# Performance work log

Hardware: AMD Instinct MI355X
Metric: run time of the kernel (lower is better)

Reference implementation:

```python
import jax, jax.numpy as jnp
import numpy as np

jax.config.update("jax_enable_x64", True)

SIGMA = 10            # STDP time window
POPULATIONS = 2
LR = 1e-3
IN_FEATURES = 1568    # populations * 28 * 28
OUT_FEATURES = 10
BATCH = 64
NUM_STEPS = 256
TWO_SIGMA = 2 * SIGMA


def _normalize(LL, prior):
    # clamp to [-7, 0], then log-normalize over population axis / over outputs
    LL = jnp.clip(LL, -7.0, 0.0)
    pf = LL.reshape(POPULATIONS, -1, OUT_FEATURES)
    LL = (pf - jax.nn.logsumexp(pf, axis=0, keepdims=True)).reshape(IN_FEATURES, OUT_FEATURES)
    prior = jnp.clip(prior, -7.0, 0.0)
    prior = prior - jax.nn.logsumexp(prior)
    return LL, prior


def _run(x, LL, prior):
    B, T, F = x.shape
    LL = LL.astype(jnp.float64)
    prior = prior.astype(jnp.float64)
    LL, prior = _normalize(LL, prior)  # __init__ calls normalize_probs()
    # Padded cumulative spike counts: Cp[:, t] = sum_{s < t} x[:, s]
    Cp = jnp.concatenate(
        [jnp.zeros((B, 1, F), jnp.int32), jnp.cumsum(x.astype(jnp.int32), axis=1)], axis=1)
    t = jnp.arange(T)
    lo = jnp.take(Cp, jnp.clip(t - SIGMA + 1, 0, T), axis=1)   # sum_{s <= t-sigma} x, (B,T,F)
    tp_sigma = jnp.take(Cp, t + 1, axis=1) - lo                # LTP trace: spikes in [t-sigma+1, t]
    tp_s2inf = lo                                              # LTD trace: spikes older than sigma
    potential = tp_sigma > 0                                   # OR of binary spikes in sigma-window
    # post_only gate: no presynaptic spike in [t+1-4*sigma, t-1]
    no_pre = (jnp.take(Cp, t, axis=1)
              - jnp.take(Cp, jnp.clip(t + 1 - 4 * SIGMA, 0, T), axis=1)) == 0

    xs = (jnp.moveaxis(x, 1, 0), jnp.moveaxis(potential, 1, 0),
          jnp.moveaxis(tp_sigma, 1, 0), jnp.moveaxis(tp_s2inf, 1, 0),
          jnp.moveaxis(no_pre, 1, 0), t)

    dt = LL.dtype
    ring0 = jnp.zeros((TWO_SIGMA, B, OUT_FEATURES), jnp.int32)
    z0 = jnp.zeros((B, OUT_FEATURES), jnp.int32)
    carry0 = (LL, prior, jnp.asarray(1.0, dt), ring0, z0, z0, jax.random.key(42))

    def step(carry, inp):
        LL, prior, decay, ring, ring_sum, cum, key = carry
        x_t, pot_t, tps_t, tps2_t, nopre_t, tt = inp
        key, sk = jax.random.split(key)
        logits = pot_t.astype(dt) @ LL + prior                  # (B, out)
        w = jax.nn.one_hot(jax.random.categorical(sk, logits, axis=-1),
                           OUT_FEATURES, dtype=dt)              # sampled winners (B, out)
        tpost = ring_sum.astype(dt)                             # post trace, winners in [t-2sig, t-1]
        tpost_inf = (cum - ring_sum).astype(dt)                 # post trace, older than 2*sigma
        ltp = jnp.einsum('bi,bo->io', tps_t.astype(dt), w)
        ltd = jnp.einsum('bi,bo->io', tps2_t.astype(dt), w)
        post_pre = jnp.einsum('bi,bo->io', x_t.astype(dt), tpost)
        post_only = jnp.einsum('bi,bo->io', nopre_t.astype(dt), tpost_inf)
        scale = LR / decay
        LL = LL + ((jnp.exp(-LL) - 1.0) * ltp - ltd - post_pre - post_only) * scale
        ps = w.sum(axis=0)
        prior = prior + ((jnp.exp(-prior) - 1.0) * ps - (1.0 - ps)) * scale
        LL, prior = _normalize(LL, prior)
        wi = w.astype(jnp.int32)
        slot = tt % TWO_SIGMA
        ring_sum = ring_sum + wi - ring[slot]
        ring = ring.at[slot].set(wi)
        cum = cum + wi
        return (LL, prior, decay + 1.0, ring, ring_sum, cum, key), wi

    (LL, prior, *_), winners = jax.lax.scan(step, carry0, xs)
    return winners, LL, prior


def setup_inputs():
    key = jax.random.key(0)
    k1, k2, k3 = jax.random.split(key, 3)
    x = jax.random.randint(k1, (BATCH, NUM_STEPS, IN_FEATURES), 0, 2, dtype=jnp.int32)
    log_likelihood = jax.random.uniform(k2, (IN_FEATURES, OUT_FEATURES), dtype=jnp.float64) * -1.0 - 1.0
    log_prior = jax.random.uniform(k3, (OUT_FEATURES,), dtype=jnp.float64) * -1.0 - 1.0
    return {"x": x, "log_likelihood": log_likelihood, "log_prior": log_prior}


def reference(x, log_likelihood, log_prior):
    winners, _, _ = _run(x, log_likelihood, log_prior)
    return jnp.argmax(winners.sum(axis=0), axis=-1)  # (batch,), as in the torch forward
```

## Files before the change

### kernel.cpp

```cpp
#include <hip/hip_runtime.h>
#include <stdint.h>
#include <math.h>

#define NF 1568
#define PPOP 784
#define NOUT 10
#define NB 64
#define NT 256
#define RINGN 20
#define NBLK 8
#define TPB 512
#define PSH 98
#define TSW 16
#define TCH 64
#define ICH 64
#define LDP 66

__device__ __forceinline__ uint32_t rotl32(uint32_t v, int r){ return (v<<r)|(v>>(32-r)); }

__device__ __forceinline__ void tf2x32(uint32_t k0, uint32_t k1, uint32_t x0, uint32_t x1,
                                       uint32_t& o0, uint32_t& o1){
  uint32_t ks2 = k0 ^ k1 ^ 0x1BD11BDAu;
  x0 += k0; x1 += k1;
#define TF_RND(r) { x0 += x1; x1 = rotl32(x1,(r)); x1 ^= x0; }
  TF_RND(13) TF_RND(15) TF_RND(26) TF_RND(6)
  x0 += k1;  x1 += ks2 + 1u;
  TF_RND(17) TF_RND(29) TF_RND(16) TF_RND(24)
  x0 += ks2; x1 += k0 + 2u;
  TF_RND(13) TF_RND(15) TF_RND(26) TF_RND(6)
  x0 += k0;  x1 += k1 + 3u;
  TF_RND(17) TF_RND(29) TF_RND(16) TF_RND(24)
  x0 += k1;  x1 += ks2 + 4u;
  TF_RND(13) TF_RND(15) TF_RND(26) TF_RND(6)
  x0 += ks2; x1 += k0 + 5u;
#undef TF_RND
  o0 = x0; o1 = x1;
}

__global__ void kInit(const float* __restrict__ prior_in, double* __restrict__ prior,
                      uint32_t* __restrict__ sk){
  int tid = threadIdx.x;
  if (tid == 0){
    uint32_t k0 = 0u, k1 = 42u;
    for (int t = 0; t < NT; t++){
      uint32_t a,b; tf2x32(k0,k1,0u,1u,a,b); sk[2*t] = a; sk[2*t+1] = b;
      uint32_t c,d; tf2x32(k0,k1,0u,0u,c,d); k0 = c; k1 = d;
    }
  }
  if (tid == 1){
    double v[NOUT];
    double m = -1e300;
    for (int o = 0; o < NOUT; o++){
      double p = (double)prior_in[o];
      p = fmin(0.0, fmax(-7.0, p));
      v[o] = p; m = fmax(m, p);
    }
    double s = 0.0;
    for (int o = 0; o < NOUT; o++) s += exp(v[o]-m);
    double lse = log(s) + m;
    for (int o = 0; o < NOUT; o++) prior[o] = v[o] - lse;
  }
}

__global__ void kInitLL(const float* __restrict__ LL_in, double* __restrict__ G){
  int u = blockIdx.x*256 + threadIdx.x;
  int p = u/NOUT, o = u%NOUT;
  if (p >= PPOP) return;
  double l0 = fmin(0.0, fmax(-7.0, (double)LL_in[p*NOUT+o]));
  double l1 = fmin(0.0, fmax(-7.0, (double)LL_in[(p+PPOP)*NOUT+o]));
  double m = fmax(l0,l1);
  double lse = log(exp(l0-m)+exp(l1-m)) + m;
  G[o*NF + p]        = l0 - lse;
  G[o*NF + p + PPOP] = l1 - lse;
}

__global__ void kTraceC(const int* __restrict__ x, uint16_t* __restrict__ stage,
                        uint64_t* __restrict__ hist_st, int* __restrict__ tot_st, int t0){
  int b = blockIdx.y;
  int i = blockIdx.x*256 + threadIdx.x;
  if (i >= NF) return;
  int sidx = b*NF + i;
  uint64_t hist = (t0 == 0) ? 0ull : hist_st[sidx];
  int total     = (t0 == 0) ? 0    : tot_st[sidx];
  const int* xb = x + (size_t)b*NT*NF + i;
  for (int tl = 0; tl < TCH; tl++){
    int t = t0 + tl;
    int xv = xb[(size_t)t*NF];
    hist = (hist << 1) | (uint64_t)(uint32_t)xv;
    total += xv;
    int tps  = __popcll(hist & 0x3FFull);
    int tps2 = total - tps;
    int pot  = (tps > 0) ? 1 : 0;
    int npre = ((hist & 0x000000FFFFFFFFFEull) == 0) ? 1 : 0;
    stage[((size_t)tl*NB + b)*NF + i] =
      (uint16_t)(tps | (tps2<<4) | (pot<<12) | (npre<<13) | (xv<<14));
  }
  hist_st[sidx] = hist; tot_st[sidx] = total;
}

__global__ void kPack(const uint16_t* __restrict__ stage, uint64_t* __restrict__ masks, int t0){
  __shared__ uint16_t ld[NB*LDP];
  int tl = blockIdx.y, chunk = blockIdx.x;
  int i0 = chunk*ICH;
  int tid = threadIdx.x, lane = tid & 63, wv = tid >> 6;
  for (int r = wv; r < NB; r += 4){
    int i = i0 + lane;
    ld[r*LDP + lane] = (i < NF) ? stage[((size_t)tl*NB + r)*NF + i] : (uint16_t)0;
  }
  __syncthreads();
  int t = t0 + tl;
  for (int r = 0; r < 16; r++){
    int il = wv*16 + r;
    int i = i0 + il;
    if (i >= NF) break;
    uint16_t v = ld[lane*LDP + il];
    uint64_t sel = 0;
#pragma unroll
    for (int k = 0; k < 15; k++){
      uint64_t m = __ballot(((v >> k) & 1) != 0);
      if (lane == k) sel = m;
    }
    if (lane < 15) masks[((size_t)t*16 + lane)*NF + i] = sel;
  }
}

__global__ void kGum(const uint32_t* __restrict__ sk, double* __restrict__ gum){
  int t = blockIdx.x;
  uint32_t k0 = sk[2*t], k1 = sk[2*t+1];
  for (int idx = threadIdx.x; idx < NB*NOUT; idx += blockDim.x){
    uint32_t h,l; tf2x32(k0,k1,0u,(uint32_t)idx,h,l);
    uint64_t bits = ((uint64_t)h << 32) | (uint64_t)l;
    uint64_t fb = (bits >> 12) | 0x3FF0000000000000ull;
    double u01 = __longlong_as_double((long long)fb) - 1.0;
    double u = fmax(2.2250738585072014e-308, u01);
    gum[(size_t)t*NB*NOUT + idx] = -log(-log(u));
  }
}

__device__ __forceinline__ uint32_t poll32(uint64_t* addr, uint32_t tag){
  for (;;){
    uint64_t v = __hip_atomic_load(addr, __ATOMIC_RELAXED, __HIP_MEMORY_SCOPE_AGENT);
    if ((uint32_t)(v >> 32) == tag) return (uint32_t)v;
    __builtin_amdgcn_s_sleep(1);
  }
}

__device__ __forceinline__ int shpix(int s, int j){
  return s*PSH + (j < PSH ? j : j + (PPOP - PSH));
}

__global__ void __launch_bounds__(TPB)
kFused(const uint64_t* __restrict__ masks, double* __restrict__ G,
       const double* __restrict__ prior_g, const double* __restrict__ gum,
       uint64_t* part_lo, uint64_t* part_hi, uint64_t* wslots,
       int* __restrict__ out){
  const int bid = blockIdx.x, tid = threadIdx.x;
  const int lane = tid & 63, wv = tid >> 6;

  __shared__ double LL_s[NOUT][NF];
  __shared__ uint64_t scratch[14*196];
  __shared__ double pin_s[NBLK][NOUT];
  __shared__ double red_s[8][NOUT];
  __shared__ double colsum_s[NOUT], shsum_s[NOUT];
  __shared__ double prior_s[NOUT], pv_s[NOUT];
  __shared__ double lse_sh;
  __shared__ uint64_t wm_s[NOUT];
  __shared__ uint64_t ring_s[RINGN*NOUT];
  __shared__ uint64_t TP_s[NOUT][5];
  __shared__ int ring_cnt_s[NB*NOUT];
  __shared__ int cum_s[NB*NOUT];
  __shared__ int wloc_s[8];
  __shared__ uint32_t pk_s[NBLK];
  __shared__ int wlist_s[8][64];

  uint64_t* pot_s = scratch;
  uint64_t* bst   = scratch;

  double* LLf = &LL_s[0][0];
  for (int k = tid; k < NOUT*NF; k += TPB) LLf[k] = G[k];
  if (tid < NOUT) prior_s[tid] = prior_g[tid];
  for (int k = tid; k < RINGN*NOUT; k += TPB) ring_s[k] = 0;
  for (int k = tid; k < NB*NOUT; k += TPB){ ring_cnt_s[k] = 0; cum_s[k] = 0; }
  __syncthreads();

  for (int t = 0; t < NT; t++){
    const uint32_t tag = (uint32_t)(t + 1);
    const int b = bid*8 + wv;
    const uint64_t* M0 = masks + (size_t)t*16*NF;
    const uint64_t* potrow = M0 + 12*NF;

    double gpre = (lane < NOUT) ? gum[((size_t)t*NB + b)*NOUT + lane] : 0.0;

    if (t == 0){
      double a0=0,a1=0,a2=0,a3=0,a4=0,a5=0,a6=0,a7=0,a8=0,a9=0;
      for (int i = tid; i < NF; i += TPB){
        a0+=LL_s[0][i]; a1+=LL_s[1][i]; a2+=LL_s[2][i]; a3+=LL_s[3][i]; a4+=LL_s[4][i];
        a5+=LL_s[5][i]; a6+=LL_s[6][i]; a7+=LL_s[7][i]; a8+=LL_s[8][i]; a9+=LL_s[9][i];
      }
#define WRED(x) for (int s = 32; s > 0; s >>= 1) x += __shfl_down(x, s, 64);
      WRED(a0) WRED(a1) WRED(a2) WRED(a3) WRED(a4)
      WRED(a5) WRED(a6) WRED(a7) WRED(a8) WRED(a9)
      if (lane == 0){
        red_s[wv][0]=a0; red_s[wv][1]=a1; red_s[wv][2]=a2; red_s[wv][3]=a3;
        red_s[wv][4]=a4; red_s[wv][5]=a5; red_s[wv][6]=a6; red_s[wv][7]=a7;
        red_s[wv][8]=a8; red_s[wv][9]=a9;
      }
      __syncthreads();
      if (tid < NOUT){
        double s = 0.0;
        for (int w8 = 0; w8 < 8; w8++) s += red_s[w8][tid];
        colsum_s[tid] = s;
      }
      __syncthreads();
      for (int k = tid; k < NF; k += TPB) pot_s[k] = potrow[k];
      __syncthreads();
    } else {
      if (tid < NBLK*NOUT){
        uint32_t lo = poll32(&part_lo[tid], (uint32_t)t);
        uint32_t hi = poll32(&part_hi[tid], (uint32_t)t);
        pin_s[tid/NOUT][tid%NOUT] = __longlong_as_double(((uint64_t)hi << 32) | lo);
      } else if (tid >= 128){
        for (int k = tid - 128; k < NF; k += (TPB - 128)) pot_s[k] = potrow[k];
      }
      __syncthreads();
      if (tid < NOUT){
        double s = 0.0;
        for (int w8 = 0; w8 < NBLK; w8++) s += pin_s[w8][tid];
        colsum_s[tid] = s;
      }
      if (t < TSW){
        for (int s = 0; s < NBLK; s++){
          if (s == bid) continue;
          for (int k = tid; k < 2*PSH*NOUT; k += TPB){
            int o = k/(2*PSH), r = k%(2*PSH);
            int i = shpix(s, r);
            LL_s[o][i] = __hip_atomic_load(&G[o*NF + i], __ATOMIC_RELAXED,
                                           __HIP_MEMORY_SCOPE_AGENT);
          }
        }
      }
      __syncthreads();
    }

    {
      double cadd = 0.0;
      if (t < TSW){
        for (int c = 0; c < 25; c++){
          int i = c*64 + lane;
          uint64_t word = (i < NF) ? pot_s[i] : ~0ull;
          uint64_t mm = __ballot(((word >> b) & 1ull) == 0ull);
          while (mm){
            int bb = __ffsll((unsigned long long)mm) - 1; mm &= mm - 1;
            int ii = c*64 + bb;
            if (lane < NOUT) cadd += LL_s[lane][ii];
          }
        }
      } else {
        int cnt = 0;
        for (int c = 0; c < 25; c++){
          int i = c*64 + lane;
          uint64_t word = (i < NF) ? pot_s[i] : ~0ull;
          bool z = ((word >> b) & 1ull) == 0ull;
          uint64_t mm = __ballot(z);
          if (z){
            int pos = __popcll(mm & ((1ull << lane) - 1ull));
            if (cnt + pos < 64) wlist_s[wv][cnt + pos] = i;
          }
          cnt += __popcll(mm);
          if (cnt > 64) break;
        }
        asm volatile("s_waitcnt lgkmcnt(0)" ::: "memory");
        if (cnt <= 64){
          if (lane < NOUT){
            double c0=0, c1=0, c2=0, c3=0;
            int e = 0;
            for (; e + 4 <= cnt; e += 4){
              c0 += __hip_atomic_load(&G[lane*NF + wlist_s[wv][e]],   __ATOMIC_RELAXED, __HIP_MEMORY_SCOPE_AGENT);
              c1 += __hip_atomic_load(&G[lane*NF + wlist_s[wv][e+1]], __ATOMIC_RELAXED, __HIP_MEMORY_SCOPE_AGENT);
              c2 += __hip_atomic_load(&G[lane*NF + wlist_s[wv][e+2]], __ATOMIC_RELAXED, __HIP_MEMORY_SCOPE_AGENT);
              c3 += __hip_atomic_load(&G[lane*NF + wlist_s[wv][e+3]], __ATOMIC_RELAXED, __HIP_MEMORY_SCOPE_AGENT);
            }
            for (; e < cnt; e++)
              c0 += __hip_atomic_load(&G[lane*NF + wlist_s[wv][e]],   __ATOMIC_RELAXED, __HIP_MEMORY_SCOPE_AGENT);
            cadd = ((c0 + c1) + (c2 + c3));
          }
        } else {
          for (int c = 0; c < 25; c++){
            int i = c*64 + lane;
            uint64_t word = (i < NF) ? pot_s[i] : ~0ull;
            uint64_t mm = __ballot(((word >> b) & 1ull) == 0ull);
            while (mm){
              int bb = __ffsll((unsigned long long)mm) - 1; mm &= mm - 1;
              int ii = c*64 + bb;
              if (lane < NOUT)
                cadd += __hip_atomic_load(&G[lane*NF + ii], __ATOMIC_RELAXED,
                                          __HIP_MEMORY_SCOPE_AGENT);
            }
          }
        }
      }
      double v = -1.0e308;
      if (lane < NOUT)
        v = colsum_s[lane] - cadd + prior_s[lane] + gpre;
      double best = __shfl(v, 0, 64); int w = 0;
#pragma unroll
      for (int o = 1; o < NOUT; o++){
        double vo = __shfl(v, o, 64);
        if (vo > best){ best = vo; w = o; }
      }
      if (lane == 0) wloc_s[wv] = w;
    }
    __syncthreads();

    if (wv == 0){
      if (lane == 0){
        uint32_t pk = 0;
#pragma unroll
        for (int w8 = 0; w8 < 8; w8++) pk |= ((uint32_t)wloc_s[w8] & 15u) << (w8*4);
        uint64_t* wsl = wslots + (size_t)(t & 1)*NBLK;
        __hip_atomic_store(&wsl[bid], ((uint64_t)tag << 32) | (uint64_t)pk,
                           __ATOMIC_RELAXED, __HIP_MEMORY_SCOPE_AGENT);
      }
      if (lane < NBLK){
        uint64_t* wsl = wslots + (size_t)(t & 1)*NBLK;
        pk_s[lane] = poll32(&wsl[lane], tag);
      }
      int w = (int)((pk_s[lane >> 3] >> ((lane & 7)*4)) & 15u);
#pragma unroll
      for (int o = 0; o < NOUT; o++){
        uint64_t mo = __ballot(w == o);
        if (lane == 0) wm_s[o] = mo;
      }
#pragma unroll
      for (int o = 0; o < NOUT; o++){
        int c = ring_cnt_s[lane*NOUT + o];
#pragma unroll
        for (int pl = 0; pl < 5; pl++){
          uint64_t tp = __ballot(((c >> pl) & 1) != 0);
          if (lane == 0) TP_s[o][pl] = tp;
        }
      }
    } else {
      int st = tid - 64;
      for (int k = st; k < 14*196; k += (TPB - 64)){
        int pl = k / 196, j = k % 196;
        int pid = pl + (pl >= 12 ? 1 : 0);
        bst[pl*196 + j] = M0[(size_t)pid*NF + shpix(bid, j)];
      }
    }
    __syncthreads();

    double scale = 1e-3 / (double)(t + 1);

    for (int u = tid; u < PSH*NOUT; u += TPB){
      int pr = u / NOUT, o = u % NOUT;
      int gp = bid*PSH + pr, gq = gp + PPOP;
      int pj = pr, qj = pr + 98;
      uint64_t wmv = wm_s[o];
      int ltp0 = __popcll(bst[0*196+pj]&wmv) + (__popcll(bst[1*196+pj]&wmv)<<1)
               + (__popcll(bst[2*196+pj]&wmv)<<2) + (__popcll(bst[3*196+pj]&wmv)<<3);
      int ltd0 = __popcll(bst[4*196+pj]&wmv) + (__popcll(bst[5*196+pj]&wmv)<<1)
               + (__popcll(bst[6*196+pj]&wmv)<<2) + (__popcll(bst[7*196+pj]&wmv)<<3)
               + (__popcll(bst[8*196+pj]&wmv)<<4) + (__popcll(bst[9*196+pj]&wmv)<<5)
               + (__popcll(bst[10*196+pj]&wmv)<<6) + (__popcll(bst[11*196+pj]&wmv)<<7);
      int ltp1 = __popcll(bst[0*196+qj]&wmv) + (__popcll(bst[1*196+qj]&wmv)<<1)
               + (__popcll(bst[2*196+qj]&wmv)<<2) + (__popcll(bst[3*196+qj]&wmv)<<3);
      int ltd1 = __popcll(bst[4*196+qj]&wmv) + (__popcll(bst[5*196+qj]&wmv)<<1)
               + (__popcll(bst[6*196+qj]&wmv)<<2) + (__popcll(bst[7*196+qj]&wmv)<<3)
               + (__popcll(bst[8*196+qj]&wmv)<<4) + (__popcll(bst[9*196+qj]&wmv)<<5)
               + (__popcll(bst[10*196+qj]&wmv)<<6) + (__popcll(bst[11*196+qj]&wmv)<<7);
      uint64_t A13 = bst[12*196+pj], A14 = bst[13*196+pj];
      uint64_t B13 = bst[12*196+qj], B14 = bst[13*196+qj];
      int pp0 = 0, pp1 = 0;
#pragma unroll
      for (int pl = 0; pl < 5; pl++){
        uint64_t tp = TP_s[o][pl];
        pp0 += __popcll(A14 & tp) << pl;
        pp1 += __popcll(B14 & tp) << pl;
      }
      int po0 = 0, po1 = 0;
      if (t >= 21 && (A13 | B13)){
        uint64_t mm = A13;
        while (mm){
          int bb = __ffsll((unsigned long long)mm) - 1; mm &= mm - 1;
          po0 += cum_s[bb*NOUT + o] - ring_cnt_s[bb*NOUT + o];
        }
        mm = B13;
        while (mm){
          int bb = __ffsll((unsigned long long)mm) - 1; mm &= mm - 1;
          po1 += cum_s[bb*NOUT + o] - ring_cnt_s[bb*NOUT + o];
        }
      }
      double l0 = LL_s[o][gp], l1 = LL_s[o][gq];
      l0 = l0 + ((exp(-l0)-1.0)*(double)ltp0 - (double)ltd0 - (double)pp0 - (double)po0)*scale;
      l1 = l1 + ((exp(-l1)-1.0)*(double)ltp1 - (double)ltd1 - (double)pp1 - (double)po1)*scale;
      l0 = fmin(0.0, fmax(-7.0, l0));
      l1 = fmin(0.0, fmax(-7.0, l1));
      double m = fmax(l0, l1);
      double lse = log(exp(l0-m)+exp(l1-m)) + m;
      LL_s[o][gp] = l0 - lse;
      LL_s[o][gq] = l1 - lse;
    }
    __syncthreads();

    int slot = t % RINGN;
    if (tid < 256){
      for (int k = tid; k < 2*PSH*NOUT; k += 256){
        int o = k/(2*PSH), r = k%(2*PSH);
        int i = shpix(bid, r);
        __hip_atomic_store(&G[o*NF + i], LL_s[o][i], __ATOMIC_RELAXED, __HIP_MEMORY_SCOPE_AGENT);
      }
      double s0=0,s1=0,s2=0,s3=0,s4=0,s5=0,s6=0,s7=0,s8=0,s9=0;
      if (tid < 2*PSH){
        int i = shpix(bid, tid);
        s0=LL_s[0][i]; s1=LL_s[1][i]; s2=LL_s[2][i]; s3=LL_s[3][i]; s4=LL_s[4][i];
        s5=LL_s[5][i]; s6=LL_s[6][i]; s7=LL_s[7][i]; s8=LL_s[8][i]; s9=LL_s[9][i];
      }
      WRED(s0) WRED(s1) WRED(s2) WRED(s3) WRED(s4)
      WRED(s5) WRED(s6) WRED(s7) WRED(s8) WRED(s9)
#undef WRED
      if (lane == 0){
        red_s[wv][0]=s0; red_s[wv][1]=s1; red_s[wv][2]=s2; red_s[wv][3]=s3;
        red_s[wv][4]=s4; red_s[wv][5]=s5; red_s[wv][6]=s6; red_s[wv][7]=s7;
        red_s[wv][8]=s8; red_s[wv][9]=s9;
      }
      asm volatile("s_waitcnt vmcnt(0)" ::: "memory");
    } else {
      for (int k = tid - 256; k < NB*NOUT; k += 256){
        int bb = k / NOUT, oo = k % NOUT;
        int nbit = (int)((wm_s[oo] >> bb) & 1ull);
        int obit = (int)((ring_s[slot*NOUT + oo] >> bb) & 1ull);
        ring_cnt_s[k] += nbit - obit;
        cum_s[k]      += nbit;
      }
      if (tid >= 256 && tid < 256 + NOUT){
        int o = tid - 256;
        double ps = (double)__popcll(wm_s[o]);
        double pr = prior_s[o];
        pr = pr + ((exp(-pr)-1.0)*ps - (1.0-ps))*scale;
        pr = fmin(0.0, fmax(-7.0, pr));
        pv_s[o] = pr;
      }
    }
    __syncthreads();

    if (tid < NOUT){
      double s = 0.0;
      for (int w8 = 0; w8 < 4; w8++) s += red_s[w8][tid];
      shsum_s[tid] = s;
    }
    if (tid == 32){
      double m = pv_s[0];
      for (int o = 1; o < NOUT; o++) m = fmax(m, pv_s[o]);
      double s = 0.0;
      for (int o = 0; o < NOUT; o++) s += exp(pv_s[o]-m);
      lse_sh = log(s) + m;
    }
    if (tid >= 16 && tid < 16 + NOUT)
      ring_s[slot*NOUT + (tid-16)] = wm_s[tid-16];
    __syncthreads();

    if (tid < 2*NOUT){
      int o = tid >> 1, half = tid & 1;
      uint64_t bits = (uint64_t)__double_as_longlong(shsum_s[o]);
      uint32_t w32 = half ? (uint32_t)(bits >> 32) : (uint32_t)bits;
      uint64_t* dst = half ? &part_hi[bid*NOUT + o] : &part_lo[bid*NOUT + o];
      __hip_atomic_store(dst, ((uint64_t)tag << 32) | (uint64_t)w32,
                         __ATOMIC_RELAXED, __HIP_MEMORY_SCOPE_AGENT);
    }
    if (tid >= 32 && tid < 32 + NOUT)
      prior_s[tid-32] = pv_s[tid-32] - lse_sh;
    __syncthreads();
  }

  if (bid == 0 && tid < NB){
    int best = cum_s[tid*NOUT]; int w = 0;
    for (int o = 1; o < NOUT; o++){
      int v = cum_s[tid*NOUT + o];
      if (v > best){ best = v; w = o; }
    }
    out[tid] = w;
  }
}

static inline size_t alignup(size_t v){ return (v + 255) & ~(size_t)255; }

extern "C" void kernel_launch(void* const* d_in, const int* in_sizes, int n_in,
                              void* d_out, int out_size, void* d_ws, size_t ws_size,
                              hipStream_t stream){
  (void)in_sizes; (void)n_in; (void)out_size; (void)ws_size;
  const int*   x        = (const int*)d_in[0];
  const float* LL_in    = (const float*)d_in[1];
  const float* prior_in = (const float*)d_in[2];
  int* out = (int*)d_out;

  char* ws = (char*)d_ws;
  size_t off = 0;
  uint64_t* masks   = (uint64_t*)(ws + off); off += alignup((size_t)NT*16*NF*sizeof(uint64_t));
  uint16_t* stage   = (uint16_t*)(ws + off); off += alignup((size_t)TCH*NB*NF*sizeof(uint16_t));
  uint64_t* hist_st = (uint64_t*)(ws + off); off += alignup((size_t)NB*NF*sizeof(uint64_t));
  int*      tot_st  = (int*)(ws + off);      off += alignup((size_t)NB*NF*sizeof(int));
  double*   G       = (double*)(ws + off);   off += alignup((size_t)NOUT*NF*sizeof(double));
  double*   prior   = (double*)(ws + off);   off += alignup(NOUT*sizeof(double));
  uint32_t* sk      = (uint32_t*)(ws + off); off += alignup(NT*2*sizeof(uint32_t));
  double*   gum     = (double*)(ws + off);   off += alignup((size_t)NT*NB*NOUT*sizeof(double));
  uint64_t* part_lo = (uint64_t*)(ws + off); off += alignup((size_t)NBLK*NOUT*sizeof(uint64_t));
  uint64_t* part_hi = (uint64_t*)(ws + off); off += alignup((size_t)NBLK*NOUT*sizeof(uint64_t));
  uint64_t* wslots  = (uint64_t*)(ws + off); off += alignup((size_t)2*NBLK*sizeof(uint64_t));

  kInit<<<1, 256, 0, stream>>>(prior_in, prior, sk);
  kInitLL<<<31, 256, 0, stream>>>(LL_in, G);
  for (int c = 0; c < NT/TCH; c++){
    kTraceC<<<dim3((NF+255)/256, NB), 256, 0, stream>>>(x, stage, hist_st, tot_st, c*TCH);
    kPack<<<dim3((NF+ICH-1)/ICH, TCH), 256, 0, stream>>>(stage, masks, c*TCH);
  }
  kGum<<<NT, 256, 0, stream>>>(sk, gum);

  kFused<<<NBLK, TPB, 0, stream>>>(masks, G, prior, gum, part_lo, part_hi, wslots, out);
}
```

Baseline: 4.632 ms.

## Publish partial sums before G writeback and gate G reads on new mslots flags

Moves the per-block column-sum publication ahead of the global LL writeback, so the next step's colsum polling no longer waits on the G stores. A separate per-block flag array (mslots) now signals when a block's G shard is fully written. Readers poll those flags only when they actually need to read G, either for the early-step shard copy or for sparse zero-bit gathers. The aim is to take the G store latency off the cross-block critical path, at the cost of an extra flag store and extra polling.

```diff
diff --git a/kernel.cpp b/kernel.cpp
--- a/kernel.cpp
+++ b/kernel.cpp
@@ -152,7 +152,7 @@
 __global__ void __launch_bounds__(TPB)
 kFused(const uint64_t* __restrict__ masks, double* __restrict__ G,
        const double* __restrict__ prior_g, const double* __restrict__ gum,
-       uint64_t* part_lo, uint64_t* part_hi, uint64_t* wslots,
+       uint64_t* part_lo, uint64_t* part_hi, uint64_t* wslots, uint64_t* mslots,
        int* __restrict__ out){
   const int bid = blockIdx.x, tid = threadIdx.x;
   const int lane = tid & 63, wv = tid >> 6;
@@ -161,7 +161,7 @@
   __shared__ uint64_t scratch[14*196];
   __shared__ double pin_s[NBLK][NOUT];
   __shared__ double red_s[8][NOUT];
-  __shared__ double colsum_s[NOUT], shsum_s[NOUT];
+  __shared__ double colsum_s[NOUT];
   __shared__ double prior_s[NOUT], pv_s[NOUT];
   __shared__ double lse_sh;
   __shared__ uint64_t wm_s[NOUT];
@@ -229,6 +229,8 @@
         colsum_s[tid] = s;
       }
       if (t < TSW){
+        if (tid >= 16 && tid < 16 + NBLK) poll32(&mslots[tid-16], (uint32_t)t);
+        __syncthreads();
         for (int s = 0; s < NBLK; s++){
           if (s == bid) continue;
           for (int k = tid; k < 2*PSH*NOUT; k += TPB){
@@ -270,31 +272,34 @@
           if (cnt > 64) break;
         }
         asm volatile("s_waitcnt lgkmcnt(0)" ::: "memory");
-        if (cnt <= 64){
-          if (lane < NOUT){
-            double c0=0, c1=0, c2=0, c3=0;
-            int e = 0;
-            for (; e + 4 <= cnt; e += 4){
-              c0 += __hip_atomic_load(&G[lane*NF + wlist_s[wv][e]],   __ATOMIC_RELAXED, __HIP_MEMORY_SCOPE_AGENT);
-              c1 += __hip_atomic_load(&G[lane*NF + wlist_s[wv][e+1]], __ATOMIC_RELAXED, __HIP_MEMORY_SCOPE_AGENT);
-              c2 += __hip_atomic_load(&G[lane*NF + wlist_s[wv][e+2]], __ATOMIC_RELAXED, __HIP_MEMORY_SCOPE_AGENT);
-              c3 += __hip_atomic_load(&G[lane*NF + wlist_s[wv][e+3]], __ATOMIC_RELAXED, __HIP_MEMORY_SCOPE_AGENT);
+        if (cnt > 0){
+          if (lane < NBLK) poll32(&mslots[lane], (uint32_t)t);
+          if (cnt <= 64){
+            if (lane < NOUT){
+              double c0=0, c1=0, c2=0, c3=0;
+              int e = 0;
+              for (; e + 4 <= cnt; e += 4){
+                c0 += __hip_atomic_load(&G[lane*NF + wlist_s[wv][e]],   __ATOMIC_RELAXED, __HIP_MEMORY_SCOPE_AGENT);
+                c1 += __hip_atomic_load(&G[lane*NF + wlist_s[wv][e+1]], __ATOMIC_RELAXED, __HIP_MEMORY_SCOPE_AGENT);
+                c2 += __hip_atomic_load(&G[lane*NF + wlist_s[wv][e+2]], __ATOMIC_RELAXED, __HIP_MEMORY_SCOPE_AGENT);
+                c3 += __hip_atomic_load(&G[lane*NF + wlist_s[wv][e+3]], __ATOMIC_RELAXED, __HIP_MEMORY_SCOPE_AGENT);
+              }
+              for (; e < cnt; e++)
+                c0 += __hip_atomic_load(&G[lane*NF + wlist_s[wv][e]],   __ATOMIC_RELAXED, __HIP_MEMORY_SCOPE_AGENT);
+              cadd = ((c0 + c1) + (c2 + c3));
             }
-            for (; e < cnt; e++)
-              c0 += __hip_atomic_load(&G[lane*NF + wlist_s[wv][e]],   __ATOMIC_RELAXED, __HIP_MEMORY_SCOPE_AGENT);
-            cadd = ((c0 + c1) + (c2 + c3));
-          }
-        } else {
-          for (int c = 0; c < 25; c++){
-            int i = c*64 + lane;
-            uint64_t word = (i < NF) ? pot_s[i] : ~0ull;
-            uint64_t mm = __ballot(((word >> b) & 1ull) == 0ull);
-            while (mm){
-              int bb = __ffsll((unsigned long long)mm) - 1; mm &= mm - 1;
-              int ii = c*64 + bb;
-              if (lane < NOUT)
-                cadd += __hip_atomic_load(&G[lane*NF + ii], __ATOMIC_RELAXED,
-                                          __HIP_MEMORY_SCOPE_AGENT);
+          } else {
+            for (int c = 0; c < 25; c++){
+              int i = c*64 + lane;
+              uint64_t word = (i < NF) ? pot_s[i] : ~0ull;
+              uint64_t mm = __ballot(((word >> b) & 1ull) == 0ull);
+              while (mm){
+                int bb = __ffsll((unsigned long long)mm) - 1; mm &= mm - 1;
+                int ii = c*64 + bb;
+                if (lane < NOUT)
+                  cadd += __hip_atomic_load(&G[lane*NF + ii], __ATOMIC_RELAXED,
+                                            __HIP_MEMORY_SCOPE_AGENT);
+              }
             }
           }
         }
@@ -405,11 +410,6 @@
 
     int slot = t % RINGN;
     if (tid < 256){
-      for (int k = tid; k < 2*PSH*NOUT; k += 256){
-        int o = k/(2*PSH), r = k%(2*PSH);
-        int i = shpix(bid, r);
-        __hip_atomic_store(&G[o*NF + i], LL_s[o][i], __ATOMIC_RELAXED, __HIP_MEMORY_SCOPE_AGENT);
-      }
       double s0=0,s1=0,s2=0,s3=0,s4=0,s5=0,s6=0,s7=0,s8=0,s9=0;
       if (tid < 2*PSH){
         int i = shpix(bid, tid);
@@ -424,7 +424,6 @@
         red_s[wv][4]=s4; red_s[wv][5]=s5; red_s[wv][6]=s6; red_s[wv][7]=s7;
         red_s[wv][8]=s8; red_s[wv][9]=s9;
       }
-      asm volatile("s_waitcnt vmcnt(0)" ::: "memory");
     } else {
       for (int k = tid - 256; k < NB*NOUT; k += 256){
         int bb = k / NOUT, oo = k % NOUT;
@@ -445,9 +444,14 @@
     __syncthreads();
 
     if (tid < NOUT){
-      double s = 0.0;
-      for (int w8 = 0; w8 < 4; w8++) s += red_s[w8][tid];
-      shsum_s[tid] = s;
+      double s = red_s[0][tid] + red_s[1][tid] + red_s[2][tid] + red_s[3][tid];
+      uint64_t bits = (uint64_t)__double_as_longlong(s);
+      __hip_atomic_store(&part_lo[bid*NOUT + tid],
+                         ((uint64_t)tag << 32) | (uint64_t)(uint32_t)bits,
+                         __ATOMIC_RELAXED, __HIP_MEMORY_SCOPE_AGENT);
+      __hip_atomic_store(&part_hi[bid*NOUT + tid],
+                         ((uint64_t)tag << 32) | (uint64_t)(uint32_t)(bits >> 32),
+                         __ATOMIC_RELAXED, __HIP_MEMORY_SCOPE_AGENT);
     }
     if (tid == 32){
       double m = pv_s[0];
@@ -456,18 +460,21 @@
       for (int o = 0; o < NOUT; o++) s += exp(pv_s[o]-m);
       lse_sh = log(s) + m;
     }
-    if (tid >= 16 && tid < 16 + NOUT)
-      ring_s[slot*NOUT + (tid-16)] = wm_s[tid-16];
+    if (tid >= 48 && tid < 48 + NOUT)
+      ring_s[slot*NOUT + (tid-48)] = wm_s[tid-48];
+    if (tid >= 64 && tid < 320){
+      for (int k = tid - 64; k < 2*PSH*NOUT; k += 256){
+        int o = k/(2*PSH), r = k%(2*PSH);
+        int i = shpix(bid, r);
+        __hip_atomic_store(&G[o*NF + i], LL_s[o][i], __ATOMIC_RELAXED, __HIP_MEMORY_SCOPE_AGENT);
+      }
+      asm volatile("s_waitcnt vmcnt(0)" ::: "memory");
+    }
     __syncthreads();
 
-    if (tid < 2*NOUT){
-      int o = tid >> 1, half = tid & 1;
-      uint64_t bits = (uint64_t)__double_as_longlong(shsum_s[o]);
-      uint32_t w32 = half ? (uint32_t)(bits >> 32) : (uint32_t)bits;
-      uint64_t* dst = half ? &part_hi[bid*NOUT + o] : &part_lo[bid*NOUT + o];
-      __hip_atomic_store(dst, ((uint64_t)tag << 32) | (uint64_t)w32,
+    if (tid == 0)
+      __hip_atomic_store(&mslots[bid], ((uint64_t)tag << 32),
                          __ATOMIC_RELAXED, __HIP_MEMORY_SCOPE_AGENT);
-    }
     if (tid >= 32 && tid < 32 + NOUT)
       prior_s[tid-32] = pv_s[tid-32] - lse_sh;
     __syncthreads();
@@ -507,6 +514,7 @@
   uint64_t* part_lo = (uint64_t*)(ws + off); off += alignup((size_t)NBLK*NOUT*sizeof(uint64_t));
   uint64_t* part_hi = (uint64_t*)(ws + off); off += alignup((size_t)NBLK*NOUT*sizeof(uint64_t));
   uint64_t* wslots  = (uint64_t*)(ws + off); off += alignup((size_t)2*NBLK*sizeof(uint64_t));
+  uint64_t* mslots  = (uint64_t*)(ws + off); off += alignup((size_t)NBLK*sizeof(uint64_t));
 
   kInit<<<1, 256, 0, stream>>>(prior_in, prior, sk);
   kInitLL<<<31, 256, 0, stream>>>(LL_in, G);
@@ -516,5 +524,6 @@
   }
   kGum<<<NT, 256, 0, stream>>>(sk, gum);
 
-  kFused<<<NBLK, TPB, 0, stream>>>(masks, G, prior, gum, part_lo, part_hi, wslots, out);
-}
+  kFused<<<NBLK, TPB, 0, stream>>>(masks, G, prior, gum, part_lo, part_hi, wslots,
+                                   mslots, out);
+}
```

Result: no change. 4.645 ms (+0.3%).
